# Kernel optimization log

Measured on AMD Instinct MI355X. Metric: run time of the kernel, lower is better.

The kernel has to match this reference:

```python
import jax, jax.numpy as jnp
import numpy as np

N, E = 100000, 1600000
IN_C, HID, HEADS, OUT_C = 128, 32, 4, 2
NEG_SLOPE = 0.2


def _gat_layer(x, src, dst, W, a_src, a_dst, b, n_nodes, heads, c):
    # x: [N, F_in] -> h: [N, H, C]
    h = (x @ W).reshape(n_nodes, heads, c)
    alpha_s = jnp.sum(h * a_src, axis=-1)  # [N, H]
    alpha_d = jnp.sum(h * a_dst, axis=-1)  # [N, H]
    e = jax.nn.leaky_relu(alpha_s[src] + alpha_d[dst], NEG_SLOPE)  # [E, H]
    # segment softmax over incoming edges of each dst node
    m = jax.ops.segment_max(e, dst, num_segments=n_nodes)  # [N, H]
    ee = jnp.exp(e - m[dst])
    denom = jax.ops.segment_sum(ee, dst, num_segments=n_nodes)  # [N, H]
    alpha = ee / (denom[dst] + 1e-16)  # [E, H]
    out = jax.ops.segment_sum(h[src] * alpha[:, :, None], dst, num_segments=n_nodes)  # [N, H, C]
    return out.reshape(n_nodes, heads * c) + b


def _gat_forward(x, edge_index, W1, a_src1, a_dst1, b1, W2, a_src2, a_dst2, b2, Wfc, bfc):
    n = x.shape[0]
    loops = jnp.arange(n, dtype=edge_index.dtype)
    src = jnp.concatenate([edge_index[0], loops])  # PyG adds self-loops
    dst = jnp.concatenate([edge_index[1], loops])
    h = jax.nn.elu(_gat_layer(x, src, dst, W1, a_src1, a_dst1, b1, n, HEADS, HID))
    h = jax.nn.elu(_gat_layer(h, src, dst, W2, a_src2, a_dst2, b2, n, HEADS, HID))
    return h @ Wfc + bfc


def setup_inputs() -> dict:
    key = jax.random.key(0)
    ks = jax.random.split(key, 12)
    g = lambda k, shape, fan: jax.random.normal(k, shape, jnp.float32) * (1.0 / np.sqrt(fan))
    return {
        "x": jax.random.normal(ks[0], (N, IN_C), jnp.float32),
        "edge_index": jax.random.randint(ks[1], (2, E), 0, N, jnp.int64),
        "W1": g(ks[2], (IN_C, HEADS * HID), IN_C),
        "a_src1": g(ks[3], (HEADS, HID), HID),
        "a_dst1": g(ks[4], (HEADS, HID), HID),
        "b1": jnp.zeros((HEADS * HID,), jnp.float32),
        "W2": g(ks[5], (HEADS * HID, HEADS * HID), HEADS * HID),
        "a_src2": g(ks[6], (HEADS, HID), HID),
        "a_dst2": g(ks[7], (HEADS, HID), HID),
        "b2": jnp.zeros((HEADS * HID,), jnp.float32),
        "Wfc": g(ks[8], (HEADS * HID, OUT_C), HEADS * HID),
        "bfc": jnp.zeros((OUT_C,), jnp.float32),
    }


def reference(x, edge_index, W1, a_src1, a_dst1, b1, W2, a_src2, a_dst2, b2, Wfc, bfc):
    return _gat_forward(x, edge_index, W1, a_src1, a_dst1, b1, W2, a_src2, a_dst2, b2, Wfc, bfc)
```

## Files before the change

kernel.cpp:

```cpp
#include <hip/hip_runtime.h>
#include <hip/hip_fp16.h>
#include <math.h>

#define FEAT 128
#define NBLK 256
#define BSHIFT 8

typedef _Float16 f16x8 __attribute__((ext_vector_type(8)));
typedef float f32x4 __attribute__((ext_vector_type(4)));

__device__ __forceinline__ float eluf(float x) {
  return x > 0.0f ? x : (__expf(x) - 1.0f);
}
__device__ __forceinline__ float lreluf(float x) {
  return x > 0.0f ? x : 0.2f * x;
}


__global__ __launch_bounds__(256) void scan1_kernel(const int* __restrict__ cnt,
                                                    int* __restrict__ pre,
                                                    int* __restrict__ bsum, int n) {
  __shared__ int sd[256];
  const int t = threadIdx.x;
  const int idx = blockIdx.x * 1024 + t * 4;
  int4 v = make_int4(0, 0, 0, 0);
  if (idx + 3 < n) {
    v = *(const int4*)(cnt + idx);
  } else {
    if (idx < n)     v.x = cnt[idx];
    if (idx + 1 < n) v.y = cnt[idx + 1];
    if (idx + 2 < n) v.z = cnt[idx + 2];
    if (idx + 3 < n) v.w = cnt[idx + 3];
  }
  const int tsum = v.x + v.y + v.z + v.w;
  sd[t] = tsum;
  __syncthreads();
  for (int o = 1; o < 256; o <<= 1) {
    int x = (t >= o) ? sd[t - o] : 0;
    __syncthreads();
    sd[t] += x;
    __syncthreads();
  }
  const int excl = sd[t] - tsum;
  if (idx < n)     pre[idx]     = excl;
  if (idx + 1 < n) pre[idx + 1] = excl + v.x;
  if (idx + 2 < n) pre[idx + 2] = excl + v.x + v.y;
  if (idx + 3 < n) pre[idx + 3] = excl + v.x + v.y + v.z;
  if (t == 255) bsum[blockIdx.x] = sd[255];
}

__global__ __launch_bounds__(256) void scan2_kernel(int* __restrict__ bsum, int nb) {
  __shared__ int sd[256];
  const int t = threadIdx.x;
  int v = (t < nb) ? bsum[t] : 0;
  sd[t] = v;
  __syncthreads();
  for (int o = 1; o < 256; o <<= 1) {
    int x = (t >= o) ? sd[t - o] : 0;
    __syncthreads();
    sd[t] += x;
    __syncthreads();
  }
  if (t < nb) bsum[t] = sd[t] - v;
}

__global__ __launch_bounds__(256) void bucket_hist_kernel(
    const int* __restrict__ ei, int* __restrict__ gh,
    int E, int ET, int nbuck, int chunk) {
  __shared__ int h[512];
  const int t = threadIdx.x;
  const int b = blockIdx.x;
  h[t] = 0; h[t + 256] = 0;
  __syncthreads();
  const int lo = b * chunk;
  const int hi = min(lo + chunk, ET);
  for (int i = lo + t; i < hi; i += 256) {
    int d = (i < E) ? ei[E + i] : (i - E);
    atomicAdd(&h[d >> BSHIFT], 1);
  }
  __syncthreads();
  for (int k = t; k < nbuck; k += 256) gh[k * NBLK + b] = h[k];
}

__global__ __launch_bounds__(256) void bucket_scatter_kernel(
    const int* __restrict__ ei, const int* __restrict__ ghp,
    const int* __restrict__ bsum, int2* __restrict__ pairs,
    int E, int ET, int nbuck, int chunk) {
  __shared__ int cur[512];
  const int t = threadIdx.x;
  const int b = blockIdx.x;
  for (int k = t; k < nbuck; k += 256) {
    int idx = k * NBLK + b;
    cur[k] = ghp[idx] + bsum[idx >> 10];
  }
  __syncthreads();
  const int lo = b * chunk;
  const int hi = min(lo + chunk, ET);
  for (int i = lo + t; i < hi; i += 256) {
    int s, d;
    if (i < E) { s = ei[i]; d = ei[E + i]; } else { s = d = i - E; }
    int pos = atomicAdd(&cur[d >> BSHIFT], 1);
    pairs[pos] = make_int2(s, d);
  }
}

__global__ __launch_bounds__(256) void bucket_finalize_kernel(
    const int2* __restrict__ pairs, const int* __restrict__ ghp,
    const int* __restrict__ bsum, int* __restrict__ row_ptr,
    int* __restrict__ esrc, int N, int ET, int nbuck) {
  __shared__ int hist[256];
  __shared__ int cur[256];
  const int t = threadIdx.x;
  const int k = blockIdx.x;
  const int node0 = k << BSHIFT;
  const int idx0 = k * NBLK;
  const int base = ghp[idx0] + bsum[idx0 >> 10];
  int end;
  if (k + 1 < nbuck) {
    const int idx1 = (k + 1) * NBLK;
    end = ghp[idx1] + bsum[idx1 >> 10];
  } else {
    end = ET;
  }
  hist[t] = 0;
  __syncthreads();
  for (int e = base + t; e < end; e += 256) {
    atomicAdd(&hist[pairs[e].y - node0], 1);
  }
  __syncthreads();
  const int v = hist[t];
  __syncthreads();
  __shared__ int sd[256];
  sd[t] = v;
  __syncthreads();
  for (int o = 1; o < 256; o <<= 1) {
    int x = (t >= o) ? sd[t - o] : 0;
    __syncthreads();
    sd[t] += x;
    __syncthreads();
  }
  const int excl = sd[t] - v;
  if (node0 + t < N) row_ptr[node0 + t] = base + excl;
  cur[t] = excl;
  __syncthreads();
  for (int e = base + t; e < end; e += 256) {
    int2 p = pairs[e];
    int pos = atomicAdd(&cur[p.y - node0], 1);
    esrc[base + pos] = p.x;
  }
  if (k == 0 && t == 0) row_ptr[N] = ET;
}

__global__ __launch_bounds__(256) void pack_w_kernel(
    const float* __restrict__ W, const float* __restrict__ a_src,
    const float* __restrict__ a_dst, __half* __restrict__ frag) {
  int tid = blockIdx.x * 256 + threadIdx.x;
  if (tid >= 4 * 9 * 64) return;
  int lane = tid & 63;
  int tile = (tid >> 6) % 9;
  int ks = tid / (9 * 64);
  int li = lane & 15, hi = lane >> 4;
  int col = tile * 16 + li;
  __half* dst = frag + (size_t)tid * 8;
  for (int i = 0; i < 8; ++i) {
    int k = ks * 32 + hi * 8 + i;
    float v = 0.f;
    if (col < 128) {
      v = W[k * 128 + col];
    } else if (col < 132) {
      int h = col - 128;
      float s = 0.f;
      for (int j = 0; j < 32; ++j) s += W[k * 128 + h * 32 + j] * a_src[h * 32 + j];
      v = s;
    } else if (col < 136) {
      int h = col - 132;
      float s = 0.f;
      for (int j = 0; j < 32; ++j) s += W[k * 128 + h * 32 + j] * a_dst[h * 32 + j];
      v = s;
    }
    dst[i] = __float2half(v);
  }
}

template <bool F32IN>
__global__ __launch_bounds__(256) void gemm_mfma_kernel(
    const void* __restrict__ in, const __half* __restrict__ frag,
    __half* __restrict__ hout, float* __restrict__ as_out, float* __restrict__ ad_out,
    int nrows) {
  const int wid = (blockIdx.x * 256 + threadIdx.x) >> 6;
  const int lane = threadIdx.x & 63;
  const int li = lane & 15, hi = lane >> 4;
  int row = wid * 16 + li;
  const bool valid = row < nrows;
  if (wid * 16 >= nrows) return;
  if (!valid) row = nrows - 1;

  const f16x8* fragv = (const f16x8*)frag;

  f32x4 acc[9];
#pragma unroll
  for (int t = 0; t < 9; ++t) acc[t] = (f32x4){0.f, 0.f, 0.f, 0.f};

#pragma unroll
  for (int ks = 0; ks < 4; ++ks) {
    f16x8 xf;
    if (F32IN) {
      const float* xp = (const float*)in + (size_t)row * FEAT + ks * 32 + hi * 8;
      float4 v0 = *(const float4*)xp;
      float4 v1 = *(const float4*)(xp + 4);
      xf[0] = (_Float16)v0.x; xf[1] = (_Float16)v0.y;
      xf[2] = (_Float16)v0.z; xf[3] = (_Float16)v0.w;
      xf[4] = (_Float16)v1.x; xf[5] = (_Float16)v1.y;
      xf[6] = (_Float16)v1.z; xf[7] = (_Float16)v1.w;
    } else {
      xf = *(const f16x8*)((const __half*)in + (size_t)row * FEAT + ks * 32 + hi * 8);
    }
#pragma unroll
    for (int t = 0; t < 9; ++t) {
      f16x8 wf = fragv[(ks * 9 + t) * 64 + lane];
      acc[t] = __builtin_amdgcn_mfma_f32_16x16x32_f16(wf, xf, acc[t], 0, 0, 0);
    }
  }

  if (!valid) return;
#pragma unroll
  for (int t = 0; t < 8; ++t) {
    union { __half2 h[2]; uint2 u; } pk;
    pk.h[0] = __floats2half2_rn(acc[t][0], acc[t][1]);
    pk.h[1] = __floats2half2_rn(acc[t][2], acc[t][3]);
    *(uint2*)(hout + (size_t)row * FEAT + t * 16 + hi * 4) = pk.u;
  }
  if (hi == 0) *(float4*)(as_out + row * 4) = make_float4(acc[8][0], acc[8][1], acc[8][2], acc[8][3]);
  if (hi == 1) *(float4*)(ad_out + row * 4) = make_float4(acc[8][0], acc[8][1], acc[8][2], acc[8][3]);
}

__global__ __launch_bounds__(256) void node_gat_kernel(
    const int* __restrict__ row_ptr, const int* __restrict__ esrc,
    const float* __restrict__ as_, const float* __restrict__ ad_,
    const __half2* __restrict__ h, const float* __restrict__ bias,
    __half2* __restrict__ out16, float* __restrict__ outf, int n) {
  const int wid = (blockIdx.x * 256 + threadIdx.x) >> 6;
  if (wid >= n) return;
  const int l = threadIdx.x & 63;
  const int begin = row_ptr[wid];
  const int end = row_ptr[wid + 1];
  const int hd = l >> 4;
  const float adv = ad_[wid * 4 + hd];

  float2 a2 = make_float2(0.f, 0.f);
  float den = 0.f;
  int e = begin;
  for (; e + 3 < end; e += 4) {
    const int s0 = esrc[e + 0];
    const int s1 = esrc[e + 1];
    const int s2 = esrc[e + 2];
    const int s3 = esrc[e + 3];
    const float w0 = __expf(lreluf(as_[s0 * 4 + hd] + adv));
    const float w1 = __expf(lreluf(as_[s1 * 4 + hd] + adv));
    const float w2 = __expf(lreluf(as_[s2 * 4 + hd] + adv));
    const float w3 = __expf(lreluf(as_[s3 * 4 + hd] + adv));
    const float2 h0 = __half22float2(h[(size_t)s0 * 64 + l]);
    const float2 h1 = __half22float2(h[(size_t)s1 * 64 + l]);
    const float2 h2 = __half22float2(h[(size_t)s2 * 64 + l]);
    const float2 h3 = __half22float2(h[(size_t)s3 * 64 + l]);
    den += (w0 + w1) + (w2 + w3);
    a2.x = fmaf(h0.x, w0, a2.x);
    a2.y = fmaf(h0.y, w0, a2.y);
    a2.x = fmaf(h1.x, w1, a2.x);
    a2.y = fmaf(h1.y, w1, a2.y);
    a2.x = fmaf(h2.x, w2, a2.x);
    a2.y = fmaf(h2.y, w2, a2.y);
    a2.x = fmaf(h3.x, w3, a2.x);
    a2.y = fmaf(h3.y, w3, a2.y);
  }
  for (; e < end; ++e) {
    const int s0 = esrc[e];
    const float w0 = __expf(lreluf(as_[s0 * 4 + hd] + adv));
    const float2 h0 = __half22float2(h[(size_t)s0 * 64 + l]);
    den += w0;
    a2.x = fmaf(h0.x, w0, a2.x);
    a2.y = fmaf(h0.y, w0, a2.y);
  }
  const float inv = 1.0f / (den + 1e-16f);
  const float o0 = a2.x * inv;
  const float o1 = a2.y * inv;
  if (out16) {
    const float2 b = *(const float2*)(bias + l * 2);
    out16[(size_t)wid * 64 + l] = __floats2half2_rn(eluf(o0 + b.x), eluf(o1 + b.y));
  } else {
    outf[(size_t)wid * FEAT + l * 2 + 0] = o0;
    outf[(size_t)wid * FEAT + l * 2 + 1] = o1;
  }
}

__global__ __launch_bounds__(256) void fc_kernel(
    const float* __restrict__ acc, const float* __restrict__ bias,
    const float* __restrict__ Wfc, const float* __restrict__ bfc,
    float* __restrict__ out, int n) {
  __shared__ float wl[256];
  __shared__ float bl[128];
  const int t = threadIdx.x;
  wl[t] = Wfc[t & 255];
  if (t < 128) bl[t] = bias[t];
  __syncthreads();
  int idx = blockIdx.x * 256 + t;
  int node = idx >> 5;
  int l = idx & 31;
  if (node >= n) return;
  float4 v = *(const float4*)(acc + (size_t)node * FEAT + l * 4);
  float h0 = eluf(v.x + bl[l * 4 + 0]);
  float h1 = eluf(v.y + bl[l * 4 + 1]);
  float h2 = eluf(v.z + bl[l * 4 + 2]);
  float h3 = eluf(v.w + bl[l * 4 + 3]);
  float s0 = h0 * wl[(l * 4 + 0) * 2 + 0] + h1 * wl[(l * 4 + 1) * 2 + 0] +
             h2 * wl[(l * 4 + 2) * 2 + 0] + h3 * wl[(l * 4 + 3) * 2 + 0];
  float s1 = h0 * wl[(l * 4 + 0) * 2 + 1] + h1 * wl[(l * 4 + 1) * 2 + 1] +
             h2 * wl[(l * 4 + 2) * 2 + 1] + h3 * wl[(l * 4 + 3) * 2 + 1];
#pragma unroll
  for (int o = 16; o >= 1; o >>= 1) {
    s0 += __shfl_xor(s0, o);
    s1 += __shfl_xor(s1, o);
  }
  if (l == 0) {
    out[node * 2 + 0] = s0 + bfc[0];
    out[node * 2 + 1] = s1 + bfc[1];
  }
}

extern "C" void kernel_launch(void* const* d_in, const int* in_sizes, int n_in,
                              void* d_out, int out_size, void* d_ws, size_t ws_size,
                              hipStream_t stream) {
  const float* x   = (const float*)d_in[0];
  const int*   ei  = (const int*)d_in[1];
  const float* W1  = (const float*)d_in[2];
  const float* as1 = (const float*)d_in[3];
  const float* ad1 = (const float*)d_in[4];
  const float* b1  = (const float*)d_in[5];
  const float* W2  = (const float*)d_in[6];
  const float* as2 = (const float*)d_in[7];
  const float* ad2 = (const float*)d_in[8];
  const float* b2  = (const float*)d_in[9];
  const float* Wfc = (const float*)d_in[10];
  const float* bfc = (const float*)d_in[11];
  float* out = (float*)d_out;

  const int N = in_sizes[0] / FEAT;
  const int E = in_sizes[1] / 2;
  const int ET = E + N;
  const int nbuck = (N + 255) >> BSHIFT;
  const int NN = nbuck * NBLK;
  const int chunk = (ET + NBLK - 1) / NBLK;

  char* ws = (char*)d_ws;
  __half* hraw = (__half*)ws;
  __half* hin2 = hraw + (size_t)N * FEAT;
  float* acc   = (float*)(hin2 + (size_t)N * FEAT);
  float* asb   = acc + (size_t)N * FEAT;
  float* adb   = asb + (size_t)N * 4;
  __half* bfrag1 = (__half*)(adb + (size_t)N * 4);
  __half* bfrag2 = bfrag1 + 4 * 9 * 64 * 8;
  int* bsum    = (int*)(bfrag2 + 4 * 9 * 64 * 8);
  int* row_ptr = bsum + 256;
  int* esrc    = row_ptr + (N + 1);
  int* gh    = (int*)acc;
  int* ghp   = gh + NN;
  int2* pairs = (int2*)(ghp + NN);

  const dim3 b256(256);
  const int nb = (NN + 1023) / 1024;

  pack_w_kernel<<<9, b256, 0, stream>>>(W1, as1, ad1, bfrag1);
  pack_w_kernel<<<9, b256, 0, stream>>>(W2, as2, ad2, bfrag2);

  bucket_hist_kernel<<<NBLK, b256, 0, stream>>>(ei, gh, E, ET, nbuck, chunk);
  scan1_kernel<<<nb, b256, 0, stream>>>(gh, ghp, bsum, NN);
  scan2_kernel<<<1, b256, 0, stream>>>(bsum, nb);
  bucket_scatter_kernel<<<NBLK, b256, 0, stream>>>(ei, ghp, bsum, pairs, E, ET, nbuck, chunk);
  bucket_finalize_kernel<<<nbuck, b256, 0, stream>>>(pairs, ghp, bsum, row_ptr, esrc, N, ET, nbuck);

  const int ntiles = (N + 15) / 16;
  const int ggrid = (ntiles + 3) / 4;
  const int wgrid = (N * 64 + 255) / 256;
  const int fgrid = (N * 32 + 255) / 256;

  gemm_mfma_kernel<true><<<ggrid, b256, 0, stream>>>(x, bfrag1, hraw, asb, adb, N);
  node_gat_kernel<<<wgrid, b256, 0, stream>>>(row_ptr, esrc, asb, adb,
                                              (const __half2*)hraw, b1,
                                              (__half2*)hin2, nullptr, N);

  gemm_mfma_kernel<false><<<ggrid, b256, 0, stream>>>(hin2, bfrag2, hraw, asb, adb, N);
  node_gat_kernel<<<wgrid, b256, 0, stream>>>(row_ptr, esrc, asb, adb,
                                              (const __half2*)hraw, nullptr,
                                              nullptr, acc, N);

  fc_kernel<<<fgrid, b256, 0, stream>>>(acc, b2, Wfc, bfc, out, N);
}
```

Baseline: 294.6 us.

## Fuse FC into second GAT aggregation, pack edge pairs, unroll gather by 8

Folds the final ELU and the 128-to-2 linear layer into the second node aggregation kernel using a wave-wide shuffle reduction. This removes the fc kernel launch and the full float accumulator write and re-read. Edge pairs in the CSR build are packed into one 32-bit word (source shifted left by 8 plus the low 8 bits of the destination), which halves the scatter and finalize traffic. The gather loop is unrolled to 8 edges with all loads issued before use, which raises memory-level parallelism at some register cost.

Measured after the change: 268.5 us. 8.8% less time.

```diff
diff --git a/kernel.cpp b/kernel.cpp
--- a/kernel.cpp
+++ b/kernel.cpp
@@ -11,9 +11,6 @@
 
 __device__ __forceinline__ float eluf(float x) {
   return x > 0.0f ? x : (__expf(x) - 1.0f);
-}
-__device__ __forceinline__ float lreluf(float x) {
-  return x > 0.0f ? x : 0.2f * x;
 }
 
 
@@ -84,7 +81,7 @@
 
 __global__ __launch_bounds__(256) void bucket_scatter_kernel(
     const int* __restrict__ ei, const int* __restrict__ ghp,
-    const int* __restrict__ bsum, int2* __restrict__ pairs,
+    const int* __restrict__ bsum, unsigned* __restrict__ pairs,
     int E, int ET, int nbuck, int chunk) {
   __shared__ int cur[512];
   const int t = threadIdx.x;
@@ -100,16 +97,17 @@
     int s, d;
     if (i < E) { s = ei[i]; d = ei[E + i]; } else { s = d = i - E; }
     int pos = atomicAdd(&cur[d >> BSHIFT], 1);
-    pairs[pos] = make_int2(s, d);
+    pairs[pos] = ((unsigned)s << 8) | (unsigned)(d & 255);
   }
 }
 
 __global__ __launch_bounds__(256) void bucket_finalize_kernel(
-    const int2* __restrict__ pairs, const int* __restrict__ ghp,
+    const unsigned* __restrict__ pairs, const int* __restrict__ ghp,
     const int* __restrict__ bsum, int* __restrict__ row_ptr,
     int* __restrict__ esrc, int N, int ET, int nbuck) {
   __shared__ int hist[256];
   __shared__ int cur[256];
+  __shared__ int sd[256];
   const int t = threadIdx.x;
   const int k = blockIdx.x;
   const int node0 = k << BSHIFT;
@@ -125,12 +123,11 @@
   hist[t] = 0;
   __syncthreads();
   for (int e = base + t; e < end; e += 256) {
-    atomicAdd(&hist[pairs[e].y - node0], 1);
+    atomicAdd(&hist[pairs[e] & 255u], 1);
   }
   __syncthreads();
   const int v = hist[t];
   __syncthreads();
-  __shared__ int sd[256];
   sd[t] = v;
   __syncthreads();
   for (int o = 1; o < 256; o <<= 1) {
@@ -144,9 +141,9 @@
   cur[t] = excl;
   __syncthreads();
   for (int e = base + t; e < end; e += 256) {
-    int2 p = pairs[e];
-    int pos = atomicAdd(&cur[p.y - node0], 1);
-    esrc[base + pos] = p.x;
+    unsigned p = pairs[e];
+    int pos = atomicAdd(&cur[p & 255u], 1);
+    esrc[base + pos] = (int)(p >> 8);
   }
   if (k == 0 && t == 0) row_ptr[N] = ET;
 }
@@ -234,11 +231,13 @@
   if (hi == 1) *(float4*)(ad_out + row * 4) = make_float4(acc[8][0], acc[8][1], acc[8][2], acc[8][3]);
 }
 
+template <int MODE>
 __global__ __launch_bounds__(256) void node_gat_kernel(
     const int* __restrict__ row_ptr, const int* __restrict__ esrc,
     const float* __restrict__ as_, const float* __restrict__ ad_,
     const __half2* __restrict__ h, const float* __restrict__ bias,
-    __half2* __restrict__ out16, float* __restrict__ outf, int n) {
+    __half2* __restrict__ out16, const float* __restrict__ fcw,
+    const float* __restrict__ fcb, float* __restrict__ outf, int n) {
   const int wid = (blockIdx.x * 256 + threadIdx.x) >> 6;
   if (wid >= n) return;
   const int l = threadIdx.x & 63;
@@ -250,80 +249,75 @@
   float2 a2 = make_float2(0.f, 0.f);
   float den = 0.f;
   int e = begin;
+
+  for (; e + 7 < end; e += 8) {
+    int s[8];
+#pragma unroll
+    for (int i = 0; i < 8; ++i) s[i] = esrc[e + i];
+    float as8[8];
+#pragma unroll
+    for (int i = 0; i < 8; ++i) as8[i] = as_[s[i] * 4 + hd];
+    float2 hv[8];
+#pragma unroll
+    for (int i = 0; i < 8; ++i) hv[i] = __half22float2(h[(size_t)s[i] * 64 + l]);
+#pragma unroll
+    for (int i = 0; i < 8; ++i) {
+      const float x = as8[i] + adv;
+      const float w = __expf(fmaxf(x, 0.2f * x));
+      den += w;
+      a2.x = fmaf(hv[i].x, w, a2.x);
+      a2.y = fmaf(hv[i].y, w, a2.y);
+    }
+  }
   for (; e + 3 < end; e += 4) {
-    const int s0 = esrc[e + 0];
-    const int s1 = esrc[e + 1];
-    const int s2 = esrc[e + 2];
-    const int s3 = esrc[e + 3];
-    const float w0 = __expf(lreluf(as_[s0 * 4 + hd] + adv));
-    const float w1 = __expf(lreluf(as_[s1 * 4 + hd] + adv));
-    const float w2 = __expf(lreluf(as_[s2 * 4 + hd] + adv));
-    const float w3 = __expf(lreluf(as_[s3 * 4 + hd] + adv));
-    const float2 h0 = __half22float2(h[(size_t)s0 * 64 + l]);
-    const float2 h1 = __half22float2(h[(size_t)s1 * 64 + l]);
-    const float2 h2 = __half22float2(h[(size_t)s2 * 64 + l]);
-    const float2 h3 = __half22float2(h[(size_t)s3 * 64 + l]);
-    den += (w0 + w1) + (w2 + w3);
-    a2.x = fmaf(h0.x, w0, a2.x);
-    a2.y = fmaf(h0.y, w0, a2.y);
-    a2.x = fmaf(h1.x, w1, a2.x);
-    a2.y = fmaf(h1.y, w1, a2.y);
-    a2.x = fmaf(h2.x, w2, a2.x);
-    a2.y = fmaf(h2.y, w2, a2.y);
-    a2.x = fmaf(h3.x, w3, a2.x);
-    a2.y = fmaf(h3.y, w3, a2.y);
+    int s[4];
+#pragma unroll
+    for (int i = 0; i < 4; ++i) s[i] = esrc[e + i];
+    float as4[4];
+#pragma unroll
+    for (int i = 0; i < 4; ++i) as4[i] = as_[s[i] * 4 + hd];
+    float2 hv[4];
+#pragma unroll
+    for (int i = 0; i < 4; ++i) hv[i] = __half22float2(h[(size_t)s[i] * 64 + l]);
+#pragma unroll
+    for (int i = 0; i < 4; ++i) {
+      const float x = as4[i] + adv;
+      const float w = __expf(fmaxf(x, 0.2f * x));
+      den += w;
+      a2.x = fmaf(hv[i].x, w, a2.x);
+      a2.y = fmaf(hv[i].y, w, a2.y);
+    }
   }
   for (; e < end; ++e) {
     const int s0 = esrc[e];
-    const float w0 = __expf(lreluf(as_[s0 * 4 + hd] + adv));
+    const float x = as_[s0 * 4 + hd] + adv;
+    const float w = __expf(fmaxf(x, 0.2f * x));
     const float2 h0 = __half22float2(h[(size_t)s0 * 64 + l]);
-    den += w0;
-    a2.x = fmaf(h0.x, w0, a2.x);
-    a2.y = fmaf(h0.y, w0, a2.y);
-  }
+    den += w;
+    a2.x = fmaf(h0.x, w, a2.x);
+    a2.y = fmaf(h0.y, w, a2.y);
+  }
+
   const float inv = 1.0f / (den + 1e-16f);
   const float o0 = a2.x * inv;
   const float o1 = a2.y * inv;
-  if (out16) {
-    const float2 b = *(const float2*)(bias + l * 2);
+  const float2 b = *(const float2*)(bias + l * 2);
+  if (MODE == 0) {
     out16[(size_t)wid * 64 + l] = __floats2half2_rn(eluf(o0 + b.x), eluf(o1 + b.y));
   } else {
-    outf[(size_t)wid * FEAT + l * 2 + 0] = o0;
-    outf[(size_t)wid * FEAT + l * 2 + 1] = o1;
-  }
-}
-
-__global__ __launch_bounds__(256) void fc_kernel(
-    const float* __restrict__ acc, const float* __restrict__ bias,
-    const float* __restrict__ Wfc, const float* __restrict__ bfc,
-    float* __restrict__ out, int n) {
-  __shared__ float wl[256];
-  __shared__ float bl[128];
-  const int t = threadIdx.x;
-  wl[t] = Wfc[t & 255];
-  if (t < 128) bl[t] = bias[t];
-  __syncthreads();
-  int idx = blockIdx.x * 256 + t;
-  int node = idx >> 5;
-  int l = idx & 31;
-  if (node >= n) return;
-  float4 v = *(const float4*)(acc + (size_t)node * FEAT + l * 4);
-  float h0 = eluf(v.x + bl[l * 4 + 0]);
-  float h1 = eluf(v.y + bl[l * 4 + 1]);
-  float h2 = eluf(v.z + bl[l * 4 + 2]);
-  float h3 = eluf(v.w + bl[l * 4 + 3]);
-  float s0 = h0 * wl[(l * 4 + 0) * 2 + 0] + h1 * wl[(l * 4 + 1) * 2 + 0] +
-             h2 * wl[(l * 4 + 2) * 2 + 0] + h3 * wl[(l * 4 + 3) * 2 + 0];
-  float s1 = h0 * wl[(l * 4 + 0) * 2 + 1] + h1 * wl[(l * 4 + 1) * 2 + 1] +
-             h2 * wl[(l * 4 + 2) * 2 + 1] + h3 * wl[(l * 4 + 3) * 2 + 1];
-#pragma unroll
-  for (int o = 16; o >= 1; o >>= 1) {
-    s0 += __shfl_xor(s0, o);
-    s1 += __shfl_xor(s1, o);
-  }
-  if (l == 0) {
-    out[node * 2 + 0] = s0 + bfc[0];
-    out[node * 2 + 1] = s1 + bfc[1];
+    const float e0 = eluf(o0 + b.x);
+    const float e1 = eluf(o1 + b.y);
+    const float4 w4 = *(const float4*)(fcw + l * 4);
+    float s0 = e0 * w4.x + e1 * w4.z;
+    float s1 = e0 * w4.y + e1 * w4.w;
+#pragma unroll
+    for (int o = 32; o >= 1; o >>= 1) {
+      s0 += __shfl_xor(s0, o);
+      s1 += __shfl_xor(s1, o);
+    }
+    if (l == 0) {
+      *(float2*)(outf + (size_t)wid * 2) = make_float2(s0 + fcb[0], s1 + fcb[1]);
+    }
   }
 }
 
@@ -364,7 +358,7 @@
   int* esrc    = row_ptr + (N + 1);
   int* gh    = (int*)acc;
   int* ghp   = gh + NN;
-  int2* pairs = (int2*)(ghp + NN);
+  unsigned* pairs = (unsigned*)(ghp + NN);
 
   const dim3 b256(256);
   const int nb = (NN + 1023) / 1024;
@@ -381,17 +375,14 @@
   const int ntiles = (N + 15) / 16;
   const int ggrid = (ntiles + 3) / 4;
   const int wgrid = (N * 64 + 255) / 256;
-  const int fgrid = (N * 32 + 255) / 256;
 
   gemm_mfma_kernel<true><<<ggrid, b256, 0, stream>>>(x, bfrag1, hraw, asb, adb, N);
-  node_gat_kernel<<<wgrid, b256, 0, stream>>>(row_ptr, esrc, asb, adb,
-                                              (const __half2*)hraw, b1,
-                                              (__half2*)hin2, nullptr, N);
+  node_gat_kernel<0><<<wgrid, b256, 0, stream>>>(row_ptr, esrc, asb, adb,
+                                                 (const __half2*)hraw, b1,
+                                                 (__half2*)hin2, nullptr, nullptr, nullptr, N);
 
   gemm_mfma_kernel<false><<<ggrid, b256, 0, stream>>>(hin2, bfrag2, hraw, asb, adb, N);
-  node_gat_kernel<<<wgrid, b256, 0, stream>>>(row_ptr, esrc, asb, adb,
-                                              (const __half2*)hraw, nullptr,
-                                              nullptr, acc, N);
-
-  fc_kernel<<<fgrid, b256, 0, stream>>>(acc, b2, Wfc, bfc, out, N);
-}
+  node_gat_kernel<1><<<wgrid, b256, 0, stream>>>(row_ptr, esrc, asb, adb,
+                                                 (const __half2*)hraw, b2,
+                                                 nullptr, Wfc, bfc, out, N);
+}
```
